# Performance work log

Measured on AMD Instinct MI355X. Metric: run time of the kernel, lower is better.

## Reference

```python
import jax, jax.numpy as jnp
import numpy as np

L = 16            # num_levels
F = 2             # features per level
T = 1 << 19       # hashmap size
BASE = 16         # base resolution
RES = 512         # desired_resolution (outer trilinear grid)
N_PTS = 262144

# 8 corner offsets of a unit cube, [8,3]
OFFS = np.array([[(c >> 0) & 1, (c >> 1) & 1, (c >> 2) & 1] for c in range(8)], dtype=np.uint32)
OFFS_J = jnp.asarray(OFFS)
OFFS_B = jnp.asarray(OFFS.astype(bool))
P1 = jnp.uint32(2654435761)
P2 = jnp.uint32(805459861)


def hash_encode(x01, table):
    """Instant-NGP multiresolution hash encoding. x01: [N,3] in [0,1]. table: [L,T,F]."""
    feats = []
    for l in range(L):
        res = BASE * (2 ** l)
        pos = x01 * res                      # [N,3]
        p0 = jnp.floor(pos)
        frac = pos - p0                      # [N,3]
        corners = p0.astype(jnp.uint32)[:, None, :] + OFFS_J[None]   # [N,8,3]
        if (res + 1) ** 3 <= T:              # dense level
            c = jnp.minimum(corners, jnp.uint32(res))
            idx = c[..., 0] + c[..., 1] * jnp.uint32(res + 1) + c[..., 2] * jnp.uint32((res + 1) * (res + 1))
        else:                                # hashed level (spatial hash, xor of primes)
            idx = corners[..., 0] ^ (corners[..., 1] * P1) ^ (corners[..., 2] * P2)
            idx = idx & jnp.uint32(T - 1)
        g = table[l][idx.astype(jnp.int32)]  # [N,8,F]
        w = jnp.where(OFFS_B[None], frac[:, None, :], 1.0 - frac[:, None, :]).prod(-1)  # [N,8]
        feats.append(jnp.einsum('nc,ncf->nf', w, g))
    return jnp.concatenate(feats, axis=-1)   # [N, L*F]


def mlp(x, W0, W1, W2):
    h = jax.nn.relu(x @ W0)
    h = jax.nn.relu(h @ W1)
    return h @ W2


def setup_inputs() -> dict:
    key = jax.random.key(0)
    k1, k2, k3, k4, k5 = jax.random.split(key, 5)
    xyz = jax.random.uniform(k1, (N_PTS, 3), dtype=jnp.float32, minval=-1.0, maxval=1.0)
    table = jax.random.uniform(k2, (L, T, F), dtype=jnp.float32, minval=-1e-4, maxval=1e-4)
    W0 = jax.random.normal(k3, (L * F, 64), dtype=jnp.float32) * (1.0 / np.sqrt(L * F))
    W1 = jax.random.normal(k4, (64, 64), dtype=jnp.float32) * (1.0 / 8.0)
    W2 = jax.random.normal(k5, (64, 8), dtype=jnp.float32) * (1.0 / 8.0)
    return {"xyz": xyz, "table": table, "W0": W0, "W1": W1, "W2": W2, "bound": 1}


def reference(xyz, table, W0, W1, W2, bound):
    xn = (xyz + bound) / (2 * bound)          # [N,3] in [0,1]
    coords = xn * RES
    c0 = jnp.clip(jnp.floor(coords), 0.0, RES - 1.0)   # [N,3] floats holding ints
    frac = coords - c0                         # u,v,w per-axis [N,3]
    out = jnp.zeros((xyz.shape[0], 8), dtype=xyz.dtype)
    for b in range(8):
        bits = np.array([(b >> 0) & 1, (b >> 1) & 1, (b >> 2) & 1], dtype=np.float32)
        cc = (c0 + bits) / RES                 # corner point normalized to [0,1]
        f = mlp(hash_encode(cc, table), W0, W1, W2)   # [N,8]
        w = jnp.where(bits.astype(bool), frac, 1.0 - frac).prod(-1)  # [N]
        out = out + w[:, None] * f
    return out
```

## Files before the change

### kernel.cpp

```cpp
#include <hip/hip_runtime.h>


typedef __attribute__((ext_vector_type(8))) short short8_t;
typedef __attribute__((ext_vector_type(4))) float f32x4;
typedef unsigned long long ull;

static constexpr unsigned kT    = 1u << 19;
static constexpr unsigned kMask = kT - 1u;
static constexpr unsigned cP1   = 2654435761u;
static constexpr unsigned cP2   = 805459861u;
static constexpr int      BLOCK = 256;
static constexpr int      TOFF  = 4096;
static constexpr unsigned D01   = 1u << 21;
static constexpr unsigned N01   = 35937u;
static constexpr unsigned D2    = D01 + 72000u;
static constexpr unsigned N2    = 274625u;
static constexpr unsigned PARTO = 2621440u;
static constexpr size_t   WS_NEED  = ((size_t)TOFF + (1u << 21)) * 4;
static constexpr size_t   WS_NEED2 = ((size_t)PARTO + (1u << 22)) * 4;

static __device__ __forceinline__ unsigned bf16_rn(float x) {
    unsigned u = __float_as_uint(x);
    return (u + 0x7fffu + ((u >> 16) & 1u)) >> 16;
}

static __device__ __forceinline__ float2 bf2dec(unsigned u) {
    return make_float2(__uint_as_float(u << 16),
                       __uint_as_float(u & 0xffff0000u));
}

static __device__ __forceinline__ unsigned cvtpk(float lo, float hi) {
    unsigned r;
    asm("v_cvt_pk_bf16_f32 %0, %1, %2" : "=v"(r) : "v"(lo), "v"(hi));
    return r;
}

static __device__ __forceinline__ f32x4 mfma16(short8_t a, short8_t b, f32x4 c) {
    return __builtin_amdgcn_mfma_f32_16x16x32_bf16(a, b, c, 0, 0, 0);
}

__global__ __launch_bounds__(256)
void prep_all(const float* __restrict__ W0, const float* __restrict__ W1,
              const float* __restrict__ W2, const float2* __restrict__ tbl,
              unsigned* __restrict__ ws, int ncc, int ncf, int ncd, int nc01)
{
    const int bx = blockIdx.x, tid = threadIdx.x;
    if (bx < ncc) {
        const int i = bx * 256 + tid;
        const ull* __restrict__ p = (const ull*)(tbl + (size_t)3 * kT);
        const ull a = __builtin_nontemporal_load(p + 2 * (size_t)i);
        const ull b = __builtin_nontemporal_load(p + 2 * (size_t)i + 1);
        ((ull*)(ws + TOFF))[i] =
              (ull)(bf16_rn(__uint_as_float((unsigned)a))
                  | (bf16_rn(__uint_as_float((unsigned)(a >> 32))) << 16))
            | ((ull)(bf16_rn(__uint_as_float((unsigned)b))
                  | (bf16_rn(__uint_as_float((unsigned)(b >> 32))) << 16)) << 32);
    } else if (bx < ncc + ncf) {
        const int i = (bx - ncc) * 256 + tid;
        const unsigned vv = (1u << 20) - 1u - (unsigned)i;
        const int s = __clz((int)vv) - 12;
        const unsigned fo = (1u << 20) - ((1u << 20) >> s);
        const unsigned j = (unsigned)i - fo;
        const ull e = __builtin_nontemporal_load(
            (const ull*)tbl + ((size_t)(5 + s) << 19) + ((size_t)j << s));
        ws[TOFF + (1u << 20) + i] = bf16_rn(__uint_as_float((unsigned)e))
            | (bf16_rn(__uint_as_float((unsigned)(e >> 32))) << 16);
    } else if (bx < ncc + ncf + ncd) {
        const int i = (bx - ncc - ncf) * 256 + tid;
        if (i < (int)N2) {
            const ull e = __builtin_nontemporal_load(
                (const ull*)tbl + (size_t)2 * kT + i);
            ws[TOFF + D2 + i] = bf16_rn(__uint_as_float((unsigned)e))
                | (bf16_rn(__uint_as_float((unsigned)(e >> 32))) << 16);
        }
    } else if (bx < ncc + ncf + ncd + nc01) {
        const int i = (bx - ncc - ncf - ncd) * 256 + tid;
        if (i < (int)N01) {
            const int vz = i / 1089;
            const int r  = i - vz * 1089;
            const int vy = r / 33;
            const int vx = r - vy * 33;
            const float2 f1 = tbl[(size_t)kT + i];
            const int x0 = vx >> 1, y0 = vy >> 1, z0 = vz >> 1;
            const int x1 = (x0 + 1 > 16) ? 16 : x0 + 1;
            const int y1 = (y0 + 1 > 16) ? 16 : y0 + 1;
            const int z1 = (z0 + 1 > 16) ? 16 : z0 + 1;
            const float fx = (vx & 1) ? 0.5f : 0.0f;
            const float fy = (vy & 1) ? 0.5f : 0.0f;
            const float fz = (vz & 1) ? 0.5f : 0.0f;
            const int Y0 = y0 * 17, Y1 = y1 * 17, Z0 = z0 * 289, Z1 = z1 * 289;
            const float2 g0 = tbl[x0 + Y0 + Z0], g1 = tbl[x1 + Y0 + Z0];
            const float2 g2 = tbl[x0 + Y1 + Z0], g3 = tbl[x1 + Y1 + Z0];
            const float2 g4 = tbl[x0 + Y0 + Z1], g5 = tbl[x1 + Y0 + Z1];
            const float2 g6 = tbl[x0 + Y1 + Z1], g7 = tbl[x1 + Y1 + Z1];
            const float wx1 = fx, wx0 = 1.0f - fx;
            const float wy1 = fy, wy0 = 1.0f - fy;
            const float wz1 = fz, wz0 = 1.0f - fz;
            const float w00 = wx0 * wy0, w10 = wx1 * wy0, w01 = wx0 * wy1, w11 = wx1 * wy1;
            const float a0 = w00 * wz0, a1 = w10 * wz0, a2 = w01 * wz0, a3 = w11 * wz0;
            const float a4 = w00 * wz1, a5 = w10 * wz1, a6 = w01 * wz1, a7 = w11 * wz1;
            const float f0x = a0 * g0.x + a1 * g1.x + a2 * g2.x + a3 * g3.x
                            + a4 * g4.x + a5 * g5.x + a6 * g6.x + a7 * g7.x;
            const float f0y = a0 * g0.y + a1 * g1.y + a2 * g2.y + a3 * g3.y
                            + a4 * g4.y + a5 * g5.y + a6 * g6.y + a7 * g7.y;
            ((ull*)(ws + TOFF + D01))[i] =
                (ull)cvtpk(f0x, f0y) | ((ull)cvtpk(f1.x, f1.y) << 32);
        }
    } else {
        const int t = (bx - ncc - ncf - ncd - nc01) * 4 + (tid >> 6);
        if (t >= 14) return;
        const int lane = tid & 63;
        const int n = lane & 15, q = lane >> 4;
        unsigned hi[4];
        #pragma unroll
        for (int d = 0; d < 4; ++d) {
            unsigned h2[2];
            #pragma unroll
            for (int s = 0; s < 2; ++s) {
                const int j = d * 2 + s;
                float v;
                if (t < 4) {
                    v = W0[(q * 8 + j) * 64 + t * 16 + n];
                } else {
                    const int kp = (j < 4) ? (q * 4 + j) : (16 + q * 4 + (j - 4));
                    if (t < 12) v = W1[(((t - 4) & 1) * 32 + kp) * 64 + ((t - 4) >> 1) * 16 + n];
                    else        v = (n < 8) ? W2[((t - 12) * 32 + kp) * 8 + n] : 0.0f;
                }
                h2[s] = bf16_rn(v);
            }
            hi[d] = h2[0] | (h2[1] << 16);
        }
        ((uint4*)ws)[t * 64 + lane] = make_uint4(hi[0], hi[1], hi[2], hi[3]);
    }
}

__global__ __launch_bounds__(256, 8)
void ngp_pa(const float* __restrict__ xyz, const int* __restrict__ boundp,
            unsigned* __restrict__ ws)
{
    const int tid = threadIdx.x;
    const int ge  = blockIdx.x * 256 + tid;
    const int pt  = ge >> 3;
    const int b   = ge & 7;

    const float bnd = (float)boundp[0];
    const float sc  = 0.5f / bnd;
    const float pxv = __builtin_nontemporal_load(xyz + pt * 3 + 0);
    const float pyv = __builtin_nontemporal_load(xyz + pt * 3 + 1);
    const float pzv = __builtin_nontemporal_load(xyz + pt * 3 + 2);
    const float cxf = (pxv + bnd) * sc * 512.0f;
    const float cyf = (pyv + bnd) * sc * 512.0f;
    const float czf = (pzv + bnd) * sc * 512.0f;
    const float c0x = fminf(fmaxf(floorf(cxf), 0.0f), 511.0f);
    const float c0y = fminf(fmaxf(floorf(cyf), 0.0f), 511.0f);
    const float c0z = fminf(fmaxf(floorf(czf), 0.0f), 511.0f);
    const unsigned kx = (unsigned)c0x + (unsigned)(b & 1);
    const unsigned ky = (unsigned)c0y + (unsigned)((b >> 1) & 1);
    const unsigned kz = (unsigned)c0z + (unsigned)((b >> 2) & 1);

    const unsigned* __restrict__ tbx = ws + TOFF;
    unsigned gH[2][8];
    #pragma unroll
    for (int l = 3; l < 5; ++l) {
        const int d = 5 - l;
        const unsigned qx = kx >> d, qy = ky >> d, qz = kz >> d;
        const unsigned hy0 = qy * cP1, hy1 = hy0 + cP1;
        const unsigned hz0 = qz * cP2, hz1 = hz0 + cP2;
        const unsigned x1u = qx + 1u;
        unsigned hidx[8];
        hidx[0] = (qx  ^ hy0 ^ hz0) & kMask;  hidx[1] = (x1u ^ hy0 ^ hz0) & kMask;
        hidx[2] = (qx  ^ hy1 ^ hz0) & kMask;  hidx[3] = (x1u ^ hy1 ^ hz0) & kMask;
        hidx[4] = (qx  ^ hy0 ^ hz1) & kMask;  hidx[5] = (x1u ^ hy0 ^ hz1) & kMask;
        hidx[6] = (qx  ^ hy1 ^ hz1) & kMask;  hidx[7] = (x1u ^ hy1 ^ hz1) & kMask;
        const unsigned* __restrict__ base = tbx + (size_t)(l - 3) * kT;
        #pragma unroll
        for (int c = 0; c < 8; ++c) gH[l - 3][c] = base[hidx[c]];
    }

    unsigned xd34[2];
    #pragma unroll
    for (int l = 3; l < 5; ++l) {
        const int d = 5 - l;
        const unsigned m = (1u << d) - 1u;
        const float inv = 1.0f / (float)(1 << d);
        const float fx = (float)(kx & m) * inv;
        const float fy = (float)(ky & m) * inv;
        const float fz = (float)(kz & m) * inv;
        const float2 g0 = bf2dec(gH[l - 3][0]), g1 = bf2dec(gH[l - 3][1]);
        const float2 g2 = bf2dec(gH[l - 3][2]), g3 = bf2dec(gH[l - 3][3]);
        const float2 g4 = bf2dec(gH[l - 3][4]), g5 = bf2dec(gH[l - 3][5]);
        const float2 g6 = bf2dec(gH[l - 3][6]), g7 = bf2dec(gH[l - 3][7]);
        const float wx1 = fx, wx0 = 1.0f - fx;
        const float wy1 = fy, wy0 = 1.0f - fy;
        const float wz1 = fz, wz0 = 1.0f - fz;
        const float w00 = wx0 * wy0, w10 = wx1 * wy0, w01 = wx0 * wy1, w11 = wx1 * wy1;
        const float a0 = w00 * wz0, a1 = w10 * wz0, a2 = w01 * wz0, a3 = w11 * wz0;
        const float a4 = w00 * wz1, a5 = w10 * wz1, a6 = w01 * wz1, a7 = w11 * wz1;
        const float vx = a0 * g0.x + a1 * g1.x + a2 * g2.x + a3 * g3.x
                       + a4 * g4.x + a5 * g5.x + a6 * g6.x + a7 * g7.x;
        const float vy = a0 * g0.y + a1 * g1.y + a2 * g2.y + a3 * g3.y
                       + a4 * g4.y + a5 * g5.y + a6 * g6.y + a7 * g7.y;
        xd34[l - 3] = cvtpk(vx, vy);
    }
    ((ull*)(ws + PARTO))[ge] = (ull)xd34[0] | ((ull)xd34[1] << 32);
}

__global__ __launch_bounds__(BLOCK, 5)
void ngp_pb(const float*  __restrict__ xyz,
            const int*    __restrict__ boundp,
            const unsigned* __restrict__ wsw,
            float*        __restrict__ out)
{
    __shared__ __align__(16) unsigned lds[4096];
    const int tid  = threadIdx.x;
    const int lane = tid & 63;
    const int wv   = tid >> 6;
    const int col  = lane & 15;
    const int q    = lane >> 4;
    const int swz  = (tid ^ (tid >> 2) ^ (tid >> 4)) & 3;

    const unsigned* __restrict__ tbx = wsw + TOFF;
    const float bnd = (float)boundp[0];
    const float sc  = 0.5f / bnd;
    const f32x4 zero = {0.0f, 0.0f, 0.0f, 0.0f};

    const int ge = blockIdx.x * BLOCK + tid;
    const int pt = ge >> 3;
    const int b  = ge & 7;

    const float pxv = __builtin_nontemporal_load(xyz + pt * 3 + 0);
    const float pyv = __builtin_nontemporal_load(xyz + pt * 3 + 1);
    const float pzv = __builtin_nontemporal_load(xyz + pt * 3 + 2);
    const float cxf = (pxv + bnd) * sc * 512.0f;
    const float cyf = (pyv + bnd) * sc * 512.0f;
    const float czf = (pzv + bnd) * sc * 512.0f;
    const float c0x = fminf(fmaxf(floorf(cxf), 0.0f), 511.0f);
    const float c0y = fminf(fmaxf(floorf(cyf), 0.0f), 511.0f);
    const float c0z = fminf(fmaxf(floorf(czf), 0.0f), 511.0f);
    const float frx = cxf - c0x;
    const float fry = cyf - c0y;
    const float frz = czf - c0z;

    const unsigned kx = (unsigned)c0x + (unsigned)(b & 1);
    const unsigned ky = (unsigned)c0y + (unsigned)((b >> 1) & 1);
    const unsigned kz = (unsigned)c0z + (unsigned)((b >> 2) & 1);

    const float wb = ((b & 1) ? frx : 1.0f - frx)
                   * ((b & 2) ? fry : 1.0f - fry)
                   * ((b & 4) ? frz : 1.0f - frz);

    const unsigned kyp = ky * cP1;
    const unsigned kzp = kz * cP2;
    const unsigned X   = kx ^ kyp ^ kzp;
    unsigned gfu[11];
    #pragma unroll
    for (int l = 5; l < 16; ++l) {
        const int s = l - 5;
        const unsigned base = (1u << 20) + ((1u << 20) - ((1u << 20) >> s));
        gfu[l - 5] = tbx[base + (X & (kMask >> s))];
    }

    const ull pv = ((const ull*)(wsw + PARTO))[ge];

    unsigned xd[16];
    {
        const unsigned qx = kx >> 4, qy = ky >> 4, qz = kz >> 4;
        const float fx = (float)(kx & 15u) * 0.0625f;
        const float fy = (float)(ky & 15u) * 0.0625f;
        const float fz = (float)(kz & 15u) * 0.0625f;
        const unsigned x0 = qx, x1 = (qx + 1u > 32u) ? 32u : qx + 1u;
        const unsigned y0 = qy * 33u, y1 = ((qy + 1u > 32u) ? 32u : qy + 1u) * 33u;
        const unsigned z0 = qz * 1089u, z1 = ((qz + 1u > 32u) ? 32u : qz + 1u) * 1089u;
        const uint2* __restrict__ b01 = (const uint2*)(tbx + D01);
        const uint2 h0 = b01[x0 + y0 + z0], h1 = b01[x1 + y0 + z0];
        const uint2 h2 = b01[x0 + y1 + z0], h3 = b01[x1 + y1 + z0];
        const uint2 h4 = b01[x0 + y0 + z1], h5 = b01[x1 + y0 + z1];
        const uint2 h6 = b01[x0 + y1 + z1], h7 = b01[x1 + y1 + z1];
        const float wx1 = fx, wx0 = 1.0f - fx;
        const float wy1 = fy, wy0 = 1.0f - fy;
        const float wz1 = fz, wz0 = 1.0f - fz;
        const float w00 = wx0 * wy0, w10 = wx1 * wy0, w01 = wx0 * wy1, w11 = wx1 * wy1;
        const float a0 = w00 * wz0, a1 = w10 * wz0, a2 = w01 * wz0, a3 = w11 * wz0;
        const float a4 = w00 * wz1, a5 = w10 * wz1, a6 = w01 * wz1, a7 = w11 * wz1;
        float f0x, f0y, f1x, f1y;
        float2 d;
        d = bf2dec(h0.x); f0x  = a0 * d.x; f0y  = a0 * d.y;
        d = bf2dec(h0.y); f1x  = a0 * d.x; f1y  = a0 * d.y;
        d = bf2dec(h1.x); f0x += a1 * d.x; f0y += a1 * d.y;
        d = bf2dec(h1.y); f1x += a1 * d.x; f1y += a1 * d.y;
        d = bf2dec(h2.x); f0x += a2 * d.x; f0y += a2 * d.y;
        d = bf2dec(h2.y); f1x += a2 * d.x; f1y += a2 * d.y;
        d = bf2dec(h3.x); f0x += a3 * d.x; f0y += a3 * d.y;
        d = bf2dec(h3.y); f1x += a3 * d.x; f1y += a3 * d.y;
        d = bf2dec(h4.x); f0x += a4 * d.x; f0y += a4 * d.y;
        d = bf2dec(h4.y); f1x += a4 * d.x; f1y += a4 * d.y;
        d = bf2dec(h5.x); f0x += a5 * d.x; f0y += a5 * d.y;
        d = bf2dec(h5.y); f1x += a5 * d.x; f1y += a5 * d.y;
        d = bf2dec(h6.x); f0x += a6 * d.x; f0y += a6 * d.y;
        d = bf2dec(h6.y); f1x += a6 * d.x; f1y += a6 * d.y;
        d = bf2dec(h7.x); f0x += a7 * d.x; f0y += a7 * d.y;
        d = bf2dec(h7.y); f1x += a7 * d.x; f1y += a7 * d.y;
        xd[0] = cvtpk(f0x, f0y);
        xd[1] = cvtpk(f1x, f1y);
    }
    {
        const unsigned qx = kx >> 3, qy = ky >> 3, qz = kz >> 3;
        const float fx = (float)(kx & 7u) * 0.125f;
        const float fy = (float)(ky & 7u) * 0.125f;
        const float fz = (float)(kz & 7u) * 0.125f;
        const unsigned x0 = qx, x1 = (qx + 1u > 64u) ? 64u : qx + 1u;
        const unsigned y0 = qy * 65u, y1 = ((qy + 1u > 64u) ? 64u : qy + 1u) * 65u;
        const unsigned z0 = qz * 4225u, z1 = ((qz + 1u > 64u) ? 64u : qz + 1u) * 4225u;
        const unsigned* __restrict__ b2 = tbx + D2;
        const float2 g0 = bf2dec(b2[x0 + y0 + z0]), g1 = bf2dec(b2[x1 + y0 + z0]);
        const float2 g2 = bf2dec(b2[x0 + y1 + z0]), g3 = bf2dec(b2[x1 + y1 + z0]);
        const float2 g4 = bf2dec(b2[x0 + y0 + z1]), g5 = bf2dec(b2[x1 + y0 + z1]);
        const float2 g6 = bf2dec(b2[x0 + y1 + z1]), g7 = bf2dec(b2[x1 + y1 + z1]);
        const float wx1 = fx, wx0 = 1.0f - fx;
        const float wy1 = fy, wy0 = 1.0f - fy;
        const float wz1 = fz, wz0 = 1.0f - fz;
        const float w00 = wx0 * wy0, w10 = wx1 * wy0, w01 = wx0 * wy1, w11 = wx1 * wy1;
        const float a0 = w00 * wz0, a1 = w10 * wz0, a2 = w01 * wz0, a3 = w11 * wz0;
        const float a4 = w00 * wz1, a5 = w10 * wz1, a6 = w01 * wz1, a7 = w11 * wz1;
        const float vx = a0 * g0.x + a1 * g1.x + a2 * g2.x + a3 * g3.x
                       + a4 * g4.x + a5 * g5.x + a6 * g6.x + a7 * g7.x;
        const float vy = a0 * g0.y + a1 * g1.y + a2 * g2.y + a3 * g3.y
                       + a4 * g4.y + a5 * g5.y + a6 * g6.y + a7 * g7.y;
        xd[2] = cvtpk(vx, vy);
    }
    xd[3] = (unsigned)pv;
    xd[4] = (unsigned)(pv >> 32);
    #pragma unroll
    for (int l = 5; l < 16; ++l) xd[l] = gfu[l - 5];

    {
        uint4* xrow = (uint4*)(lds + tid * 16);
        xrow[swz]     = make_uint4(xd[0],  xd[1],  xd[2],  xd[3]);
        xrow[swz ^ 1] = make_uint4(xd[4],  xd[5],  xd[6],  xd[7]);
        xrow[swz ^ 2] = make_uint4(xd[8],  xd[9],  xd[10], xd[11]);
        xrow[swz ^ 3] = make_uint4(xd[12], xd[13], xd[14], xd[15]);
    }

    asm volatile("s_waitcnt lgkmcnt(0)" ::: "memory");
    __builtin_amdgcn_sched_barrier(0);

    short8_t w[14];
    {
        const short8_t* __restrict__ wfr = (const short8_t*)wsw;
        #pragma unroll
        for (int t = 0; t < 14; ++t) w[t] = wfr[t * 64 + lane];
    }

    #pragma unroll 1
    for (int g = 0; g < 4; ++g) {
        const int ev  = wv * 64 + g * 16 + col;
        const int esw = ((ev ^ (ev >> 2) ^ (ev >> 4)) & 3) ^ q;
        const short8_t xb = *(const short8_t*)(lds + ev * 16 + esw * 4);
        const float wbv = __shfl(wb, g * 16 + col, 64);

        unsigned hp0[4], hp1[4];
        #pragma unroll
        for (int mt = 0; mt < 4; ++mt) {
            f32x4 a = mfma16(w[mt], xb, zero);
            hp0[mt] = cvtpk(fmaxf(a[0], 0.0f), fmaxf(a[1], 0.0f));
            hp1[mt] = cvtpk(fmaxf(a[2], 0.0f), fmaxf(a[3], 0.0f));
        }
        uint4 u0 = make_uint4(hp0[0], hp1[0], hp0[1], hp1[1]);
        uint4 u1 = make_uint4(hp0[2], hp1[2], hp0[3], hp1[3]);
        short8_t bk0 = *(short8_t*)&u0;
        short8_t bk1 = *(short8_t*)&u1;

        #pragma unroll
        for (int mt = 0; mt < 4; ++mt) {
            f32x4 a = mfma16(w[4 + mt * 2], bk0, zero);
            a = mfma16(w[5 + mt * 2], bk1, a);
            hp0[mt] = cvtpk(fmaxf(a[0], 0.0f), fmaxf(a[1], 0.0f));
            hp1[mt] = cvtpk(fmaxf(a[2], 0.0f), fmaxf(a[3], 0.0f));
        }
        u0 = make_uint4(hp0[0], hp1[0], hp0[1], hp1[1]);
        u1 = make_uint4(hp0[2], hp1[2], hp0[3], hp1[3]);
        bk0 = *(short8_t*)&u0;
        bk1 = *(short8_t*)&u1;

        f32x4 a3 = mfma16(w[12], bk0, zero);
        a3 = mfma16(w[13], bk1, a3);

        float v0 = wbv * a3[0], v1 = wbv * a3[1], v2 = wbv * a3[2], v3 = wbv * a3[3];
        #pragma unroll
        for (int s = 1; s < 8; s <<= 1) {
            v0 += __shfl_xor(v0, s);
            v1 += __shfl_xor(v1, s);
            v2 += __shfl_xor(v2, s);
            v3 += __shfl_xor(v3, s);
        }
        if (((lane & 7) == 0) && q < 2) {
            const int p = (blockIdx.x * BLOCK + ev) >> 3;
            ull* op = (ull*)(out + p * 8 + q * 4);
            __builtin_nontemporal_store(
                (ull)__float_as_uint(v0) | ((ull)__float_as_uint(v1) << 32), op);
            __builtin_nontemporal_store(
                (ull)__float_as_uint(v2) | ((ull)__float_as_uint(v3) << 32), op + 1);
        }
    }
}

template<bool BT>
__global__ __launch_bounds__(BLOCK, 5)
void ngp_mfma(const float*  __restrict__ xyz,
              const float2* __restrict__ tbl,
              const int*    __restrict__ boundp,
              const unsigned* __restrict__ wsw,
              float*        __restrict__ out,
              int ntiles)
{
    __shared__ __align__(16) unsigned lds[4096];
    const int tid  = threadIdx.x;
    const int lane = tid & 63;
    const int wv   = tid >> 6;
    const int col  = lane & 15;
    const int q    = lane >> 4;
    const int swz  = (tid ^ (tid >> 2) ^ (tid >> 4)) & 3;

    const unsigned* __restrict__ tbx = wsw + TOFF;
    const float bnd = (float)boundp[0];
    const float sc  = 0.5f / bnd;
    const f32x4 zero = {0.0f, 0.0f, 0.0f, 0.0f};

    const int ge = blockIdx.x * BLOCK + tid;
    const int pt = ge >> 3;
    const int b  = ge & 7;

    const float cxf = (xyz[pt * 3 + 0] + bnd) * sc * 512.0f;
    const float cyf = (xyz[pt * 3 + 1] + bnd) * sc * 512.0f;
    const float czf = (xyz[pt * 3 + 2] + bnd) * sc * 512.0f;
    const float c0x = fminf(fmaxf(floorf(cxf), 0.0f), 511.0f);
    const float c0y = fminf(fmaxf(floorf(cyf), 0.0f), 511.0f);
    const float c0z = fminf(fmaxf(floorf(czf), 0.0f), 511.0f);
    const float frx = cxf - c0x;
    const float fry = cyf - c0y;
    const float frz = czf - c0z;

    const unsigned kx = (unsigned)c0x + (unsigned)(b & 1);
    const unsigned ky = (unsigned)c0y + (unsigned)((b >> 1) & 1);
    const unsigned kz = (unsigned)c0z + (unsigned)((b >> 2) & 1);

    const float wb = ((b & 1) ? frx : 1.0f - frx)
                   * ((b & 2) ? fry : 1.0f - fry)
                   * ((b & 4) ? frz : 1.0f - frz);

    const unsigned kyp = ky * cP1;
    const unsigned kzp = kz * cP2;
    const unsigned X   = kx ^ kyp ^ kzp;
    unsigned gfu[11];
    float2   gff[11];
    #pragma unroll
    for (int l = 5; l < 16; ++l) {
        const int s = l - 5;
        if (BT) {
            const unsigned base = (1u << 20) + ((1u << 20) - ((1u << 20) >> s));
            gfu[l - 5] = tbx[base + (X & (kMask >> s))];
        } else {
            const unsigned idx = ((kx << s) ^ (kyp << s) ^ (kzp << s)) & kMask;
            gff[l - 5] = tbl[(size_t)l * kT + idx];
        }
    }

    unsigned gH[2][8];
    float2   gHf[2][8];
    #pragma unroll
    for (int l = 3; l < 5; ++l) {
        const int d = 5 - l;
        const unsigned qx = kx >> d, qy = ky >> d, qz = kz >> d;
        const unsigned hy0 = qy * cP1, hy1 = hy0 + cP1;
        const unsigned hz0 = qz * cP2, hz1 = hz0 + cP2;
        const unsigned x1u = qx + 1u;
        unsigned hidx[8];
        hidx[0] = (qx  ^ hy0 ^ hz0) & kMask;  hidx[1] = (x1u ^ hy0 ^ hz0) & kMask;
        hidx[2] = (qx  ^ hy1 ^ hz0) & kMask;  hidx[3] = (x1u ^ hy1 ^ hz0) & kMask;
        hidx[4] = (qx  ^ hy0 ^ hz1) & kMask;  hidx[5] = (x1u ^ hy0 ^ hz1) & kMask;
        hidx[6] = (qx  ^ hy1 ^ hz1) & kMask;  hidx[7] = (x1u ^ hy1 ^ hz1) & kMask;
        if (BT) {
            const unsigned* __restrict__ base = tbx + (size_t)(l - 3) * kT;
            #pragma unroll
            for (int c = 0; c < 8; ++c) gH[l - 3][c] = base[hidx[c]];
        } else {
            const float2* __restrict__ base = tbl + (size_t)l * kT;
            #pragma unroll
            for (int c = 0; c < 8; ++c) gHf[l - 3][c] = base[hidx[c]];
        }
    }

    float2 gc[5];
    #pragma unroll
    for (int l = 0; l < 5; ++l) {
        const int d = 5 - l;
        const unsigned m = (1u << d) - 1u;
        const float inv = 1.0f / (float)(1 << d);
        const unsigned qx = kx >> d, qy = ky >> d, qz = kz >> d;
        const float fx = (float)(kx & m) * inv;
        const float fy = (float)(ky & m) * inv;
        const float fz = (float)(kz & m) * inv;
        float2 g0, g1, g2, g3, g4, g5, g6, g7;
        if (l < 3) {
            const unsigned res = 16u << l;
            const unsigned R = res + 1u, R2 = R * R;
            const unsigned x0 = (qx < res ? qx : res);
            const unsigned x1 = (qx + 1u < res ? qx + 1u : res);
            const unsigned y0 = (qy < res ? qy : res) * R;
            const unsigned y1 = (qy + 1u < res ? qy + 1u : res) * R;
            const unsigned z0 = (qz < res ? qz : res) * R2;
            const unsigned z1 = (qz + 1u < res ? qz + 1u : res) * R2;
            const float2* __restrict__ base = tbl + (size_t)l * kT;
            g0 = base[x0 + y0 + z0]; g1 = base[x1 + y0 + z0];
            g2 = base[x0 + y1 + z0]; g3 = base[x1 + y1 + z0];
            g4 = base[x0 + y0 + z1]; g5 = base[x1 + y0 + z1];
            g6 = base[x0 + y1 + z1]; g7 = base[x1 + y1 + z1];
        } else if (BT) {
            g0 = bf2dec(gH[l - 3][0]); g1 = bf2dec(gH[l - 3][1]);
            g2 = bf2dec(gH[l - 3][2]); g3 = bf2dec(gH[l - 3][3]);
            g4 = bf2dec(gH[l - 3][4]); g5 = bf2dec(gH[l - 3][5]);
            g6 = bf2dec(gH[l - 3][6]); g7 = bf2dec(gH[l - 3][7]);
        } else {
            g0 = gHf[l - 3][0]; g1 = gHf[l - 3][1]; g2 = gHf[l - 3][2]; g3 = gHf[l - 3][3];
            g4 = gHf[l - 3][4]; g5 = gHf[l - 3][5]; g6 = gHf[l - 3][6]; g7 = gHf[l - 3][7];
        }
        const float wx1 = fx, wx0 = 1.0f - fx;
        const float wy1 = fy, wy0 = 1.0f - fy;
        const float wz1 = fz, wz0 = 1.0f - fz;
        const float w00 = wx0 * wy0, w10 = wx1 * wy0, w01 = wx0 * wy1, w11 = wx1 * wy1;
        const float a0 = w00 * wz0, a1 = w10 * wz0, a2 = w01 * wz0, a3 = w11 * wz0;
        const float a4 = w00 * wz1, a5 = w10 * wz1, a6 = w01 * wz1, a7 = w11 * wz1;
        float vx = a0 * g0.x + a1 * g1.x + a2 * g2.x + a3 * g3.x
                 + a4 * g4.x + a5 * g5.x + a6 * g6.x + a7 * g7.x;
        float vy = a0 * g0.y + a1 * g1.y + a2 * g2.y + a3 * g3.y
                 + a4 * g4.y + a5 * g5.y + a6 * g6.y + a7 * g7.y;
        gc[l] = make_float2(vx, vy);
    }

    unsigned xd[16];
    #pragma unroll
    for (int l = 0; l < 5; ++l)
        xd[l] = cvtpk(gc[l].x, gc[l].y);
    #pragma unroll
    for (int l = 5; l < 16; ++l) {
        if (BT) xd[l] = gfu[l - 5];
        else    xd[l] = cvtpk(gff[l - 5].x, gff[l - 5].y);
    }
    {
        uint4* xrow = (uint4*)(lds + tid * 16);
        xrow[swz]     = make_uint4(xd[0],  xd[1],  xd[2],  xd[3]);
        xrow[swz ^ 1] = make_uint4(xd[4],  xd[5],  xd[6],  xd[7]);
        xrow[swz ^ 2] = make_uint4(xd[8],  xd[9],  xd[10], xd[11]);
        xrow[swz ^ 3] = make_uint4(xd[12], xd[13], xd[14], xd[15]);
    }

    asm volatile("s_waitcnt lgkmcnt(0)" ::: "memory");
    __builtin_amdgcn_sched_barrier(0);

    short8_t w[14];
    {
        const short8_t* __restrict__ wfr = (const short8_t*)wsw;
        #pragma unroll
        for (int t = 0; t < 14; ++t) w[t] = wfr[t * 64 + lane];
    }

    #pragma unroll 1
    for (int g = 0; g < 4; ++g) {
        const int ev  = wv * 64 + g * 16 + col;
        const int esw = ((ev ^ (ev >> 2) ^ (ev >> 4)) & 3) ^ q;
        const short8_t xb = *(const short8_t*)(lds + ev * 16 + esw * 4);
        const float wbv = __shfl(wb, g * 16 + col, 64);

        unsigned hp0[4], hp1[4];
        #pragma unroll
        for (int mt = 0; mt < 4; ++mt) {
            f32x4 a = mfma16(w[mt], xb, zero);
            hp0[mt] = cvtpk(fmaxf(a[0], 0.0f), fmaxf(a[1], 0.0f));
            hp1[mt] = cvtpk(fmaxf(a[2], 0.0f), fmaxf(a[3], 0.0f));
        }
        uint4 u0 = make_uint4(hp0[0], hp1[0], hp0[1], hp1[1]);
        uint4 u1 = make_uint4(hp0[2], hp1[2], hp0[3], hp1[3]);
        short8_t bk0 = *(short8_t*)&u0;
        short8_t bk1 = *(short8_t*)&u1;

        #pragma unroll
        for (int mt = 0; mt < 4; ++mt) {
            f32x4 a = mfma16(w[4 + mt * 2], bk0, zero);
            a = mfma16(w[5 + mt * 2], bk1, a);
            hp0[mt] = cvtpk(fmaxf(a[0], 0.0f), fmaxf(a[1], 0.0f));
            hp1[mt] = cvtpk(fmaxf(a[2], 0.0f), fmaxf(a[3], 0.0f));
        }
        u0 = make_uint4(hp0[0], hp1[0], hp0[1], hp1[1]);
        u1 = make_uint4(hp0[2], hp1[2], hp0[3], hp1[3]);
        bk0 = *(short8_t*)&u0;
        bk1 = *(short8_t*)&u1;

        f32x4 a3 = mfma16(w[12], bk0, zero);
        a3 = mfma16(w[13], bk1, a3);

        float v0 = wbv * a3[0], v1 = wbv * a3[1], v2 = wbv * a3[2], v3 = wbv * a3[3];
        #pragma unroll
        for (int s = 1; s < 8; s <<= 1) {
            v0 += __shfl_xor(v0, s);
            v1 += __shfl_xor(v1, s);
            v2 += __shfl_xor(v2, s);
            v3 += __shfl_xor(v3, s);
        }
        if (((lane & 7) == 0) && q < 2) {
            const int p = (blockIdx.x * BLOCK + ev) >> 3;
            *(float4*)(out + p * 8 + q * 4) = make_float4(v0, v1, v2, v3);
        }
    }
}

extern "C" void kernel_launch(void* const* d_in, const int* in_sizes, int n_in,
                              void* d_out, int out_size, void* d_ws, size_t ws_size,
                              hipStream_t stream) {
    const float*  xyz = (const float*)d_in[0];
    const float2* tbl = (const float2*)d_in[1];
    const float*  W0  = (const float*)d_in[2];
    const float*  W1  = (const float*)d_in[3];
    const float*  W2  = (const float*)d_in[4];
    const int*    bnd = (const int*)d_in[5];
    float* out = (float*)d_out;

    const int npts   = in_sizes[0] / 3;
    const int total  = npts * 8;
    const int ntiles = total / BLOCK;

    const bool big2 = (ws_size >= WS_NEED2);
    const bool big  = (ws_size >= WS_NEED);
    const int ncc  = big ? (1 << 19) / 256 : 0;
    const int ncf  = big ? ((1 << 20) - (1 << 9)) / 256 : 0;
    const int ncd  = big2 ? (int)((N2 + 255u) / 256u) : 0;
    const int nc01 = big2 ? (int)((N01 + 255u) / 256u) : 0;

    hipLaunchKernelGGL(prep_all, dim3(ncc + ncf + ncd + nc01 + 4), dim3(256),
                       0, stream, W0, W1, W2, tbl, (unsigned*)d_ws,
                       ncc, ncf, ncd, nc01);

    if (big2) {
        hipLaunchKernelGGL(ngp_pa, dim3(total / 256), dim3(256), 0, stream,
                           xyz, bnd, (unsigned*)d_ws);
        hipLaunchKernelGGL(ngp_pb, dim3(ntiles), dim3(BLOCK), 0, stream,
                           xyz, bnd, (const unsigned*)d_ws, out);
    } else if (big) {
        hipLaunchKernelGGL(ngp_mfma<true>, dim3(ntiles), dim3(BLOCK), 0, stream,
                           xyz, tbl, bnd, (const unsigned*)d_ws, out, ntiles);
    } else {
        hipLaunchKernelGGL(ngp_mfma<false>, dim3(ntiles), dim3(BLOCK), 0, stream,
                           xyz, tbl, bnd, (const unsigned*)d_ws, out, ntiles);
    }
}
```

Baseline: 219.4 us.

## Pack hashed levels 5-7 into one 32-byte combined row per hash key

Prep now builds a combined table indexed by the low 17 bits of the shared hash X, holding the bf16 features of levels 5-7 for every upper-bit variant. The main kernel then fetches levels 5, 6 and 7 with two adjacent 16-byte loads and picks entries by X's upper bits, instead of issuing three scattered gathers. The levels 8-15 subsampled table is shrunk and re-indexed to match. This cuts random-gather transactions per sample, at the cost of a larger prep pass and a wider per-load footprint. The unused bf16-table fallback template variant is removed.

```diff
diff --git a/kernel.cpp b/kernel.cpp
--- a/kernel.cpp
+++ b/kernel.cpp
@@ -11,12 +11,13 @@
 static constexpr unsigned cP2   = 805459861u;
 static constexpr int      BLOCK = 256;
 static constexpr int      TOFF  = 4096;
-static constexpr unsigned D01   = 1u << 21;
+static constexpr unsigned CMB   = 1u << 20;
+static constexpr unsigned SMF   = 1u << 21;
+static constexpr unsigned D01   = (1u << 21) + (1u << 17);
 static constexpr unsigned N01   = 35937u;
 static constexpr unsigned D2    = D01 + 72000u;
 static constexpr unsigned N2    = 274625u;
 static constexpr unsigned PARTO = 2621440u;
-static constexpr size_t   WS_NEED  = ((size_t)TOFF + (1u << 21)) * 4;
 static constexpr size_t   WS_NEED2 = ((size_t)PARTO + (1u << 22)) * 4;
 
 static __device__ __forceinline__ unsigned bf16_rn(float x) {
@@ -35,6 +36,11 @@
     return r;
 }
 
+static __device__ __forceinline__ unsigned pkbf(ull e) {
+    return bf16_rn(__uint_as_float((unsigned)e))
+         | (bf16_rn(__uint_as_float((unsigned)(e >> 32))) << 16);
+}
+
 static __device__ __forceinline__ f32x4 mfma16(short8_t a, short8_t b, f32x4 c) {
     return __builtin_amdgcn_mfma_f32_16x16x32_bf16(a, b, c, 0, 0, 0);
 }
@@ -42,7 +48,8 @@
 __global__ __launch_bounds__(256)
 void prep_all(const float* __restrict__ W0, const float* __restrict__ W1,
               const float* __restrict__ W2, const float2* __restrict__ tbl,
-              unsigned* __restrict__ ws, int ncc, int ncf, int ncd, int nc01)
+              unsigned* __restrict__ ws, int ncc, int ncb, int nsf, int ncd,
+              int nc01)
 {
     const int bx = blockIdx.x, tid = threadIdx.x;
     if (bx < ncc) {
@@ -50,31 +57,50 @@
         const ull* __restrict__ p = (const ull*)(tbl + (size_t)3 * kT);
         const ull a = __builtin_nontemporal_load(p + 2 * (size_t)i);
         const ull b = __builtin_nontemporal_load(p + 2 * (size_t)i + 1);
-        ((ull*)(ws + TOFF))[i] =
-              (ull)(bf16_rn(__uint_as_float((unsigned)a))
-                  | (bf16_rn(__uint_as_float((unsigned)(a >> 32))) << 16))
-            | ((ull)(bf16_rn(__uint_as_float((unsigned)b))
-                  | (bf16_rn(__uint_as_float((unsigned)(b >> 32))) << 16)) << 32);
-    } else if (bx < ncc + ncf) {
-        const int i = (bx - ncc) * 256 + tid;
-        const unsigned vv = (1u << 20) - 1u - (unsigned)i;
-        const int s = __clz((int)vv) - 12;
-        const unsigned fo = (1u << 20) - ((1u << 20) >> s);
+        ((ull*)(ws + TOFF))[i] = (ull)pkbf(a) | ((ull)pkbf(b) << 32);
+    } else if (bx < ncc + ncb) {
+        const unsigned j = (unsigned)((bx - ncc) * 256 + tid);
+        unsigned dw[8];
+        #pragma unroll
+        for (int b = 0; b < 4; ++b) {
+            const ull e = __builtin_nontemporal_load(
+                (const ull*)tbl + (size_t)5 * kT + (j | ((unsigned)b << 17)));
+            dw[b] = pkbf(e);
+        }
+        #pragma unroll
+        for (int b = 0; b < 2; ++b) {
+            const ull e = __builtin_nontemporal_load(
+                (const ull*)tbl + (size_t)6 * kT
+                + ((size_t)(j | ((unsigned)b << 17)) << 1));
+            dw[4 + b] = pkbf(e);
+        }
+        {
+            const ull e = __builtin_nontemporal_load(
+                (const ull*)tbl + (size_t)7 * kT + ((size_t)j << 2));
+            dw[6] = pkbf(e);
+            dw[7] = 0u;
+        }
+        uint4* dst = (uint4*)(ws + TOFF + CMB + j * 8);
+        dst[0] = make_uint4(dw[0], dw[1], dw[2], dw[3]);
+        dst[1] = make_uint4(dw[4], dw[5], dw[6], dw[7]);
+    } else if (bx < ncc + ncb + nsf) {
+        const int i = (bx - ncc - ncb) * 256 + tid;
+        const unsigned v = 131071u - (unsigned)i;
+        const int s = __clz((int)v) - 12;
+        const unsigned fo = (1u << 17) - (1u << (20 - s));
         const unsigned j = (unsigned)i - fo;
         const ull e = __builtin_nontemporal_load(
             (const ull*)tbl + ((size_t)(5 + s) << 19) + ((size_t)j << s));
-        ws[TOFF + (1u << 20) + i] = bf16_rn(__uint_as_float((unsigned)e))
-            | (bf16_rn(__uint_as_float((unsigned)(e >> 32))) << 16);
-    } else if (bx < ncc + ncf + ncd) {
-        const int i = (bx - ncc - ncf) * 256 + tid;
+        ws[TOFF + SMF + i] = pkbf(e);
+    } else if (bx < ncc + ncb + nsf + ncd) {
+        const int i = (bx - ncc - ncb - nsf) * 256 + tid;
         if (i < (int)N2) {
             const ull e = __builtin_nontemporal_load(
                 (const ull*)tbl + (size_t)2 * kT + i);
-            ws[TOFF + D2 + i] = bf16_rn(__uint_as_float((unsigned)e))
-                | (bf16_rn(__uint_as_float((unsigned)(e >> 32))) << 16);
-        }
-    } else if (bx < ncc + ncf + ncd + nc01) {
-        const int i = (bx - ncc - ncf - ncd) * 256 + tid;
+            ws[TOFF + D2 + i] = pkbf(e);
+        }
+    } else if (bx < ncc + ncb + nsf + ncd + nc01) {
+        const int i = (bx - ncc - ncb - nsf - ncd) * 256 + tid;
         if (i < (int)N01) {
             const int vz = i / 1089;
             const int r  = i - vz * 1089;
@@ -107,7 +133,7 @@
                 (ull)cvtpk(f0x, f0y) | ((ull)cvtpk(f1.x, f1.y) << 32);
         }
     } else {
-        const int t = (bx - ncc - ncf - ncd - nc01) * 4 + (tid >> 6);
+        const int t = (bx - ncc - ncb - nsf - ncd - nc01) * 4 + (tid >> 6);
         if (t >= 14) return;
         const int lane = tid & 63;
         const int n = lane & 15, q = lane >> 4;
@@ -252,12 +278,17 @@
     const unsigned kyp = ky * cP1;
     const unsigned kzp = kz * cP2;
     const unsigned X   = kx ^ kyp ^ kzp;
-    unsigned gfu[11];
-    #pragma unroll
-    for (int l = 5; l < 16; ++l) {
+
+    const unsigned j17 = X & ((1u << 17) - 1u);
+    const uint4 rc0 = *(const uint4*)(tbx + CMB + j17 * 8);
+    const uint4 rc1 = *(const uint4*)(tbx + CMB + j17 * 8 + 4);
+
+    unsigned gsm[8];
+    #pragma unroll
+    for (int l = 8; l < 16; ++l) {
         const int s = l - 5;
-        const unsigned base = (1u << 20) + ((1u << 20) - ((1u << 20) >> s));
-        gfu[l - 5] = tbx[base + (X & (kMask >> s))];
+        const unsigned fo = (1u << 17) - (1u << (20 - s));
+        gsm[l - 8] = tbx[SMF + fo + (X & ((1u << (19 - s)) - 1u))];
     }
 
     const ull pv = ((const ull*)(wsw + PARTO))[ge];
@@ -330,8 +361,15 @@
     }
     xd[3] = (unsigned)pv;
     xd[4] = (unsigned)(pv >> 32);
-    #pragma unroll
-    for (int l = 5; l < 16; ++l) xd[l] = gfu[l - 5];
+    {
+        const unsigned b56 = (X >> 17) & 3u;
+        xd[5] = (b56 & 2u) ? ((b56 & 1u) ? rc0.w : rc0.z)
+                           : ((b56 & 1u) ? rc0.y : rc0.x);
+        xd[6] = ((X >> 17) & 1u) ? rc1.y : rc1.x;
+        xd[7] = rc1.z;
+    }
+    #pragma unroll
+    for (int l = 8; l < 16; ++l) xd[l] = gsm[l - 8];
 
     {
         uint4* xrow = (uint4*)(lds + tid * 16);
@@ -404,7 +442,6 @@
     }
 }
 
-template<bool BT>
 __global__ __launch_bounds__(BLOCK, 5)
 void ngp_mfma(const float*  __restrict__ xyz,
               const float2* __restrict__ tbl,
@@ -421,7 +458,6 @@
     const int q    = lane >> 4;
     const int swz  = (tid ^ (tid >> 2) ^ (tid >> 4)) & 3;
 
-    const unsigned* __restrict__ tbx = wsw + TOFF;
     const float bnd = (float)boundp[0];
     const float sc  = 0.5f / bnd;
     const f32x4 zero = {0.0f, 0.0f, 0.0f, 0.0f};
@@ -450,23 +486,17 @@
 
     const unsigned kyp = ky * cP1;
     const unsigned kzp = kz * cP2;
-    const unsigned X   = kx ^ kyp ^ kzp;
-    unsigned gfu[11];
-    float2   gff[11];
+    unsigned gfu_dummy;
+    (void)gfu_dummy;
+    float2 gff[11];
     #pragma unroll
     for (int l = 5; l < 16; ++l) {
         const int s = l - 5;
-        if (BT) {
-            const unsigned base = (1u << 20) + ((1u << 20) - ((1u << 20) >> s));
-            gfu[l - 5] = tbx[base + (X & (kMask >> s))];
-        } else {
-            const unsigned idx = ((kx << s) ^ (kyp << s) ^ (kzp << s)) & kMask;
-            gff[l - 5] = tbl[(size_t)l * kT + idx];
-        }
-    }
-
-    unsigned gH[2][8];
-    float2   gHf[2][8];
+        const unsigned idx = ((kx << s) ^ (kyp << s) ^ (kzp << s)) & kMask;
+        gff[l - 5] = tbl[(size_t)l * kT + idx];
+    }
+
+    float2 gHf[2][8];
     #pragma unroll
     for (int l = 3; l < 5; ++l) {
         const int d = 5 - l;
@@ -479,15 +509,9 @@
         hidx[2] = (qx  ^ hy1 ^ hz0) & kMask;  hidx[3] = (x1u ^ hy1 ^ hz0) & kMask;
         hidx[4] = (qx  ^ hy0 ^ hz1) & kMask;  hidx[5] = (x1u ^ hy0 ^ hz1) & kMask;
         hidx[6] = (qx  ^ hy1 ^ hz1) & kMask;  hidx[7] = (x1u ^ hy1 ^ hz1) & kMask;
-        if (BT) {
-            const unsigned* __restrict__ base = tbx + (size_t)(l - 3) * kT;
-            #pragma unroll
-            for (int c = 0; c < 8; ++c) gH[l - 3][c] = base[hidx[c]];
-        } else {
-            const float2* __restrict__ base = tbl + (size_t)l * kT;
-            #pragma unroll
-            for (int c = 0; c < 8; ++c) gHf[l - 3][c] = base[hidx[c]];
-        }
+        const float2* __restrict__ base = tbl + (size_t)l * kT;
+        #pragma unroll
+        for (int c = 0; c < 8; ++c) gHf[l - 3][c] = base[hidx[c]];
     }
 
     float2 gc[5];
@@ -515,11 +539,6 @@
             g2 = base[x0 + y1 + z0]; g3 = base[x1 + y1 + z0];
             g4 = base[x0 + y0 + z1]; g5 = base[x1 + y0 + z1];
             g6 = base[x0 + y1 + z1]; g7 = base[x1 + y1 + z1];
-        } else if (BT) {
-            g0 = bf2dec(gH[l - 3][0]); g1 = bf2dec(gH[l - 3][1]);
-            g2 = bf2dec(gH[l - 3][2]); g3 = bf2dec(gH[l - 3][3]);
-            g4 = bf2dec(gH[l - 3][4]); g5 = bf2dec(gH[l - 3][5]);
-            g6 = bf2dec(gH[l - 3][6]); g7 = bf2dec(gH[l - 3][7]);
         } else {
             g0 = gHf[l - 3][0]; g1 = gHf[l - 3][1]; g2 = gHf[l - 3][2]; g3 = gHf[l - 3][3];
             g4 = gHf[l - 3][4]; g5 = gHf[l - 3][5]; g6 = gHf[l - 3][6]; g7 = gHf[l - 3][7];
@@ -542,10 +561,8 @@
     for (int l = 0; l < 5; ++l)
         xd[l] = cvtpk(gc[l].x, gc[l].y);
     #pragma unroll
-    for (int l = 5; l < 16; ++l) {
-        if (BT) xd[l] = gfu[l - 5];
-        else    xd[l] = cvtpk(gff[l - 5].x, gff[l - 5].y);
-    }
+    for (int l = 5; l < 16; ++l)
+        xd[l] = cvtpk(gff[l - 5].x, gff[l - 5].y);
     {
         uint4* xrow = (uint4*)(lds + tid * 16);
         xrow[swz]     = make_uint4(xd[0],  xd[1],  xd[2],  xd[3]);
@@ -629,26 +646,23 @@
     const int ntiles = total / BLOCK;
 
     const bool big2 = (ws_size >= WS_NEED2);
-    const bool big  = (ws_size >= WS_NEED);
-    const int ncc  = big ? (1 << 19) / 256 : 0;
-    const int ncf  = big ? ((1 << 20) - (1 << 9)) / 256 : 0;
+    const int ncc  = big2 ? (1 << 19) / 256 : 0;
+    const int ncb  = big2 ? (1 << 17) / 256 : 0;
+    const int nsf  = big2 ? 130560 / 256 : 0;
     const int ncd  = big2 ? (int)((N2 + 255u) / 256u) : 0;
     const int nc01 = big2 ? (int)((N01 + 255u) / 256u) : 0;
 
-    hipLaunchKernelGGL(prep_all, dim3(ncc + ncf + ncd + nc01 + 4), dim3(256),
-                       0, stream, W0, W1, W2, tbl, (unsigned*)d_ws,
-                       ncc, ncf, ncd, nc01);
+    hipLaunchKernelGGL(prep_all, dim3(ncc + ncb + nsf + ncd + nc01 + 4),
+                       dim3(256), 0, stream, W0, W1, W2, tbl, (unsigned*)d_ws,
+                       ncc, ncb, nsf, ncd, nc01);
 
     if (big2) {
         hipLaunchKernelGGL(ngp_pa, dim3(total / 256), dim3(256), 0, stream,
                            xyz, bnd, (unsigned*)d_ws);
         hipLaunchKernelGGL(ngp_pb, dim3(ntiles), dim3(BLOCK), 0, stream,
                            xyz, bnd, (const unsigned*)d_ws, out);
-    } else if (big) {
-        hipLaunchKernelGGL(ngp_mfma<true>, dim3(ntiles), dim3(BLOCK), 0, stream,
+    } else {
+        hipLaunchKernelGGL(ngp_mfma, dim3(ntiles), dim3(BLOCK), 0, stream,
                            xyz, tbl, bnd, (const unsigned*)d_ws, out, ntiles);
-    } else {
-        hipLaunchKernelGGL(ngp_mfma<false>, dim3(ntiles), dim3(BLOCK), 0, stream,
-                           xyz, tbl, bnd, (const unsigned*)d_ws, out, ntiles);
-    }
-}
+    }
+}
```

New measurement: 215.8 us. No clear change (-1.6%).
